# Optimization experiments

Hardware: AMD Instinct MI355X
Metric: run time of the kernel (lower is better)

The kernel has to match this reference:

```python
import jax, jax.numpy as jnp
import numpy as np

B, T, CIN = 64, 1024, 1
H1, H2 = 128, 256  # hidden sizes hardcoded in the flax module


def setup_inputs() -> dict:
    key = jax.random.key(0)
    ks = jax.random.split(key, 24)
    n = lambda k, shp: jax.random.normal(k, shp, dtype=jnp.float32) * 0.05
    z = lambda shp: jnp.zeros(shp, jnp.float32)
    return {
        "X": n(ks[0], (B, T, CIN)),
        "conv_w": n(ks[1], (4, CIN, 16)), "conv_b": z((16,)),
        # gate layout: [i, f, g, o] concatenated, as in flax LSTMCell
        "Wi1": n(ks[2], (16, 4 * H1)), "Wh1": n(ks[3], (H1, 4 * H1)), "b1": z((4 * H1,)),
        "Wi2": n(ks[4], (16, 4 * H1)), "Wh2": n(ks[5], (H1, 4 * H1)), "b2": z((4 * H1,)),
        "Wi3": n(ks[6], (2 * H1, 4 * H2)), "Wh3": n(ks[7], (H2, 4 * H2)), "b3": z((4 * H2,)),
        "Wi4": n(ks[8], (2 * H1, 4 * H2)), "Wh4": n(ks[9], (H2, 4 * H2)), "b4": z((4 * H2,)),
        "attW": n(ks[10], (2 * H2, 128)), "attWb": z((128,)),
        "attV": n(ks[11], (128, 1)), "attVb": z((1,)),
        "d1W": n(ks[12], (2 * H2, 128)), "d1b": z((128,)),
        "d2W": n(ks[13], (128, 1)), "d2b": z((1,)),
    }


def _lstm(x, Wi, Wh, b, hidden):
    """Forward-in-time LSTM over x:(B,T,D) -> outputs (B,T,hidden). flax gate order i,f,g,o."""
    Bb = x.shape[0]

    def step(carry, xt):
        c, h = carry
        z = xt @ Wi + h @ Wh + b  # (B, 4H)
        i, f, g, o = jnp.split(z, 4, axis=-1)
        c = jax.nn.sigmoid(f) * c + jax.nn.sigmoid(i) * jnp.tanh(g)
        h = jax.nn.sigmoid(o) * jnp.tanh(c)
        return (c, h), h

    init = (jnp.zeros((Bb, hidden), x.dtype), jnp.zeros((Bb, hidden), x.dtype))
    _, hs = jax.lax.scan(step, init, jnp.swapaxes(x, 0, 1))  # (T,B,H)
    return jnp.swapaxes(hs, 0, 1)


def reference(X, conv_w, conv_b, Wi1, Wh1, b1, Wi2, Wh2, b2, Wi3, Wh3, b3,
              Wi4, Wh4, b4, attW, attWb, attV, attVb, d1W, d1b, d2W, d2b):
    # Conv1d, SAME padding (flax default)
    x = jax.lax.conv_general_dilated(X, conv_w, (1,), 'SAME',
                                     dimension_numbers=('NWC', 'WIO', 'NWC')) + conv_b
    # NOTE: original flips the FEATURE axis (axis=-1), not time — reproduced faithfully
    x1 = _lstm(x, Wi1, Wh1, b1, H1)
    x2 = _lstm(jnp.flip(x, axis=-1), Wi2, Wh2, b2, H1)
    x = jnp.concatenate([x1, x2], axis=-1)  # (B,T,256)
    x3 = _lstm(x, Wi3, Wh3, b3, H2)
    x4 = _lstm(jnp.flip(x, axis=-1), Wi4, Wh4, b4, H2)
    enc = jnp.concatenate([x3, x4], axis=-1)  # (B,T,512)
    # attention pooling over time
    score = jnp.tanh(enc @ attW + attWb) @ attV + attVb  # (B,T,1)
    w = jax.nn.softmax(score, axis=1)
    ctx = jnp.sum(w * enc, axis=1)  # (B,512)
    h = jnp.tanh(ctx @ d1W + d1b)  # dropout deterministic -> identity
    return h @ d2W + d2b  # (B,1)
```

## Files before the change

kernel.cpp:

```cpp
#include <hip/hip_runtime.h>
#include <hip/hip_fp16.h>

#define B_   64
#define T_   1024
#define H1_  128
#define H2_  256
#define TC_  128
#define NCH  (T_ / TC_)
#define MCH  (B_ * TC_)

typedef unsigned int  u32;
typedef unsigned short u16;
typedef _Float16 half2_t __attribute__((ext_vector_type(2)));
typedef _Float16 half8 __attribute__((ext_vector_type(8)));
typedef float f32x4 __attribute__((ext_vector_type(4)));

__device__ __forceinline__ float fdot2(u32 w, u32 h, float acc) {
    return __builtin_amdgcn_fdot2(__builtin_bit_cast(half2_t, w),
                                  __builtin_bit_cast(half2_t, h), acc, false);
}
__device__ __forceinline__ u32 pk2(float a, float b) {
    __half2 h = __floats2half2_rn(a, b);
    return __builtin_bit_cast(u32, h);
}
__device__ __forceinline__ float hf(u16 u) { return __half2float(__builtin_bit_cast(__half, u)); }
__device__ __forceinline__ u16 fh(float f) { return __builtin_bit_cast(u16, __float2half(f)); }
__device__ __forceinline__ float sigf(float x) { return 1.0f / (1.0f + expf(-x)); }

__global__ void cvt_all(const float* __restrict__ Wh3, const float* __restrict__ Wh4,
                        const float* __restrict__ Wi3, const float* __restrict__ Wi4,
                        const float* __restrict__ attW,
                        const float* __restrict__ Wh1, const float* __restrict__ Wh2,
                        const float* __restrict__ cw, const float* __restrict__ cb,
                        const float* __restrict__ Wi1, const float* __restrict__ Wi2,
                        const float* __restrict__ b1, const float* __restrict__ b2,
                        u32* __restrict__ wpk, u32* __restrict__ wi3T,
                        u32* __restrict__ wi4T, u32* __restrict__ awT,
                        uint4* __restrict__ wpkT, u32* __restrict__ whs,
                        float* __restrict__ w4s, float* __restrict__ beffs)
{
    int idx = blockIdx.x * 256 + threadIdx.x;
    if (idx < 262144) {
        int l = idx >> 17, rem = idx & 131071, k2 = rem >> 10, j = rem & 1023;
        const float* W = l ? Wh4 : Wh3;
        wpk[idx] = pk2(W[(2 * k2) * 1024 + j], W[(2 * k2 + 1) * 1024 + j]);
    } else if (idx < 393216) {
        int rel = idx - 262144, n = rel >> 7, kp = rel & 127;
        wi3T[rel] = pk2(Wi3[(2 * kp) * 1024 + n], Wi3[(2 * kp + 1) * 1024 + n]);
    } else if (idx < 524288) {
        int rel = idx - 393216, n = rel >> 7, kp = rel & 127;
        wi4T[rel] = pk2(Wi4[(255 - 2 * kp) * 1024 + n], Wi4[(254 - 2 * kp) * 1024 + n]);
    } else if (idx < 557056) {
        int rel = idx - 524288, n = rel >> 8, kp = rel & 255;
        awT[rel] = pk2(attW[(2 * kp) * 128 + n], attW[(2 * kp + 1) * 128 + n]);
    } else if (idx < 585728) {
        int rel = idx - 557056;
        int l = rel / 14336;
        int rem = rel - l * 14336;
        int q = rem >> 10, col = rem & 1023;
        const float* W = l ? Wh4 : Wh3;
        int k2 = 72 + 4 * q;
        uint4 v;
        v.x = pk2(W[(2 * k2 + 0) * 1024 + col], W[(2 * k2 + 1) * 1024 + col]);
        v.y = pk2(W[(2 * k2 + 2) * 1024 + col], W[(2 * k2 + 3) * 1024 + col]);
        v.z = pk2(W[(2 * k2 + 4) * 1024 + col], W[(2 * k2 + 5) * 1024 + col]);
        v.w = pk2(W[(2 * k2 + 6) * 1024 + col], W[(2 * k2 + 7) * 1024 + col]);
        wpkT[rel] = v;
    } else if (idx < 651264) {
        int rel = idx - 585728;
        int l = rel >> 15, rem = rel & 32767, p = rem >> 9, col = rem & 511;
        const float* W = l ? Wh2 : Wh1;
        whs[rel] = pk2(W[(2 * p) * 512 + col], W[(2 * p + 1) * 512 + col]);
    } else if (idx < 652288) {
        int rel = idx - 651264;
        int l = rel >> 9, col = rel & 511;
        const float* Wi = l ? Wi2 : Wi1;
        const float* bb = l ? b2 : b1;
#pragma unroll
        for (int kk = 0; kk < 4; ++kk) {
            float s = 0.f;
#pragma unroll
            for (int c0 = 0; c0 < 16; ++c0) {
                int cc = l ? (15 - c0) : c0;
                s += cw[kk * 16 + c0] * Wi[cc * 512 + col];
            }
            w4s[(l * 4 + kk) * 512 + col] = s;
        }
        float be = bb[col];
#pragma unroll
        for (int c0 = 0; c0 < 16; ++c0) {
            int cc = l ? (15 - c0) : c0;
            be += cb[c0] * Wi[cc * 512 + col];
        }
        beffs[l * 512 + col] = be;
    }
}

__global__ __launch_bounds__(512) void fused_step(
    const u16* __restrict__ pre, const u32* __restrict__ wpk,
    const uint4* __restrict__ wpkT, float* __restrict__ state,
    u16* __restrict__ enc,
    const float* __restrict__ X, const u32* __restrict__ whs,
    const float* __restrict__ w4s, const float* __restrict__ beffs,
    float* __restrict__ sstC, u16* __restrict__ sstH,
    u16* __restrict__ x12, int c)
{
    __shared__ __align__(16) uint4 wlA[9][512];
    __shared__ __align__(16) uint4 wlB[9][512];
    __shared__ __align__(16) u32 hbuf_pk[128];
    __shared__ float zbuf[1024];
    __shared__ __align__(16) u32 hbs[64];

    const int j = threadIdx.x;

    if (blockIdx.x < 128) {
        if (c == 0) return;
        const int t0 = (c - 1) * TC_;
        const int blk = blockIdx.x;
        const int b = blk >> 1;
        const int layer = blk & 1;

        const u32* wp = wpk + (size_t)layer * 131072;
        u32 wrA[36], wrB[36];
#pragma unroll
        for (int q = 0; q < 36; ++q) {
            wrA[q] = wp[q * 1024 + j];
            wrB[q] = wp[q * 1024 + 512 + j];
        }
#pragma unroll
        for (int m = 0; m < 9; ++m) {
            uint4 va, vb;
            va.x = wp[(36 + 4 * m + 0) * 1024 + j];
            va.y = wp[(36 + 4 * m + 1) * 1024 + j];
            va.z = wp[(36 + 4 * m + 2) * 1024 + j];
            va.w = wp[(36 + 4 * m + 3) * 1024 + j];
            vb.x = wp[(36 + 4 * m + 0) * 1024 + 512 + j];
            vb.y = wp[(36 + 4 * m + 1) * 1024 + 512 + j];
            vb.z = wp[(36 + 4 * m + 2) * 1024 + 512 + j];
            vb.w = wp[(36 + 4 * m + 3) * 1024 + 512 + j];
            wlA[m][j] = va;
            wlB[m][j] = vb;
        }
        const uint4* wt = wpkT + (size_t)layer * 14 * 1024;

        float* st = state + ((size_t)layer * B_ + b) * 512;
        u16* hb16 = (u16*)hbuf_pk;
        float c_state = 0.f, h_last = 0.f;
        if (j < 256) {
            float h0 = (t0 == 0) ? 0.f : st[256 + j];
            c_state = (t0 == 0) ? 0.f : st[j];
            hb16[j] = fh(h0);
            h_last = h0;
        }
        __syncthreads();

        const u16* prow = pre + (size_t)(layer * MCH + b * TC_) * 1024;
        u16* encrow = enc + ((size_t)b * T_ + t0) * 512 + layer * 256;
        const uint4* hp4 = (const uint4*)hbuf_pk;

        for (int tt = 0; tt < TC_; ++tt, prow += 1024, encrow += 512) {
            u16 pA = prow[j], pB = prow[512 + j];
            float a0 = 0.f, a1 = 0.f, b0 = 0.f, b1 = 0.f;
#pragma unroll
            for (int m = 0; m < 9; ++m) {
                uint4 hh = hp4[m];
                a0 = fdot2(wrA[4 * m + 0], hh.x, a0);
                a1 = fdot2(wrA[4 * m + 1], hh.y, a1);
                a0 = fdot2(wrA[4 * m + 2], hh.z, a0);
                a1 = fdot2(wrA[4 * m + 3], hh.w, a1);
                b0 = fdot2(wrB[4 * m + 0], hh.x, b0);
                b1 = fdot2(wrB[4 * m + 1], hh.y, b1);
                b0 = fdot2(wrB[4 * m + 2], hh.z, b0);
                b1 = fdot2(wrB[4 * m + 3], hh.w, b1);
            }
#pragma unroll
            for (int m = 0; m < 9; ++m) {
                uint4 hh = hp4[9 + m];
                uint4 wa = wlA[m][j];
                uint4 wb = wlB[m][j];
                a0 = fdot2(wa.x, hh.x, a0); a1 = fdot2(wa.y, hh.y, a1);
                a0 = fdot2(wa.z, hh.z, a0); a1 = fdot2(wa.w, hh.w, a1);
                b0 = fdot2(wb.x, hh.x, b0); b1 = fdot2(wb.y, hh.y, b1);
                b0 = fdot2(wb.z, hh.z, b0); b1 = fdot2(wb.w, hh.w, b1);
            }
#pragma unroll
            for (int q = 0; q < 14; ++q) {
                uint4 hh = hp4[18 + q];
                uint4 wa = wt[q * 1024 + j];
                uint4 wb = wt[q * 1024 + 512 + j];
                a0 = fdot2(wa.x, hh.x, a0); a1 = fdot2(wa.y, hh.y, a1);
                a0 = fdot2(wa.z, hh.z, a0); a1 = fdot2(wa.w, hh.w, a1);
                b0 = fdot2(wb.x, hh.x, b0); b1 = fdot2(wb.y, hh.y, b1);
                b0 = fdot2(wb.z, hh.z, b0); b1 = fdot2(wb.w, hh.w, b1);
            }
            float zA = (a0 + a1) + hf(pA);
            float zB = (b0 + b1) + hf(pB);
            zbuf[j] = sigf(zA);
            zbuf[512 + j] = (j < 256) ? tanhf(zB) : sigf(zB);
            __syncthreads();
            if (j < 256) {
                float gi = zbuf[j], gf = zbuf[256 + j], gg = zbuf[512 + j], go = zbuf[768 + j];
                c_state = gf * c_state + gi * gg;
                float h = go * tanhf(c_state);
                hb16[j] = fh(h);
                encrow[j] = fh(h);
                h_last = h;
            }
            __syncthreads();
        }
        if (j < 256) { st[j] = c_state; st[256 + j] = h_last; }
    } else {
        if (c >= NCH) return;
        const int chain = blockIdx.x - 128;
        const int b = chain >> 1;
        const int layer = chain & 1;

        float W4[4];
#pragma unroll
        for (int kk = 0; kk < 4; ++kk) W4[kk] = w4s[(layer * 4 + kk) * 512 + j];
        float beff = beffs[layer * 512 + j];
        u32 whp[64];
#pragma unroll
        for (int p = 0; p < 64; ++p) whp[p] = whs[(layer * 64 + p) * 512 + j];

        u16* hb16 = (u16*)hbs;
        float c_state = 0.f;
        if (j < 128) {
            if (c == 0) hb16[j] = 0;
            else { c_state = sstC[chain * 128 + j]; hb16[j] = sstH[chain * 128 + j]; }
        }
        const int t0 = c * TC_;
        const float* Xb = X + (size_t)b * T_;
        float xm1 = (t0 == 0) ? 0.f : Xb[t0 - 1];
        float x0 = Xb[t0], xp1 = Xb[t0 + 1], xp2 = Xb[t0 + 2];
        __syncthreads();

        const uint4* hp4 = (const uint4*)hbs;
        u16 hprev = 0;
        for (int t = t0; t < t0 + TC_; ++t) {
            float xnext = (t + 3 < T_) ? Xb[t + 3] : 0.f;

            float za = beff + xm1 * W4[0] + x0 * W4[1] + xp1 * W4[2] + xp2 * W4[3];
            float zb = 0.f, zc = 0.f, zd = 0.f;
#pragma unroll
            for (int m = 0; m < 16; ++m) {
                uint4 hh = hp4[m];
                za = fdot2(whp[4 * m + 0], hh.x, za);
                zb = fdot2(whp[4 * m + 1], hh.y, zb);
                zc = fdot2(whp[4 * m + 2], hh.z, zc);
                zd = fdot2(whp[4 * m + 3], hh.w, zd);
            }
            float z = (za + zb) + (zc + zd);
            zbuf[j] = (j >= 256 && j < 384) ? tanhf(z) : sigf(z);
            __syncthreads();
            if (j < 128) {
                float gi = zbuf[j], gf = zbuf[128 + j], gg = zbuf[256 + j], go = zbuf[384 + j];
                c_state = gf * c_state + gi * gg;
                float h = go * tanhf(c_state);
                hprev = fh(h);
                hb16[j] = hprev;
                x12[((size_t)b * T_ + t) * 256 + layer * 128 + j] = hprev;
            }
            xm1 = x0; x0 = xp1; xp1 = xp2; xp2 = xnext;
            __syncthreads();
        }
        if (j < 128) { sstC[chain * 128 + j] = c_state; sstH[chain * 128 + j] = hprev; }
    }
}

template<int OUTMODE, int CHUNK, int LAYERED>
__global__ __launch_bounds__(256) void gemm_mfma(
    const u16* __restrict__ A, const u32* __restrict__ B0, const u32* __restrict__ B1,
    const float* __restrict__ bias0, const float* __restrict__ bias1,
    void* __restrict__ outv, int t0, int N, int K)
{
    __shared__ __align__(16) u32 Al[128][20];
    __shared__ __align__(16) u32 Bl[128][20];
    const int tid = threadIdx.x;
    const int bx = blockIdx.x;
    const int layer = LAYERED ? (bx >> 6) : 0;
    const int m0 = LAYERED ? ((bx & 63) * 128) : (bx * 128);
    const int n0 = blockIdx.y * 128;
    const u32* Bpk = layer ? B1 : B0;
    const float* bias = layer ? bias1 : bias0;
    const int K2 = K >> 1;

    const int w = tid >> 6;
    const int lane = tid & 63;
    const int wr = (w >> 1) * 64, wc = (w & 1) * 64;
    const int lr = lane & 15, lg = lane >> 4;

    f32x4 acc[4][4];
#pragma unroll
    for (int r = 0; r < 4; ++r)
#pragma unroll
        for (int c = 0; c < 4; ++c) acc[r][c] = (f32x4){0.f, 0.f, 0.f, 0.f};

    for (int k0 = 0; k0 < K; k0 += 32) {
        const int kp0 = k0 >> 1;
#pragma unroll
        for (int it = 0; it < 2; ++it) {
            int idx = tid + it * 256;
            int row = idx >> 2, q = idx & 3;
            int grow = m0 + row;
            size_t garow = CHUNK ? ((size_t)(grow >> 7) * T_ + t0 + (grow & 127)) : (size_t)grow;
            uint4 ua = *(const uint4*)(A + garow * K + k0 + q * 8);
            *(uint4*)&Al[row][q * 4] = ua;
            uint4 ub = *(const uint4*)(Bpk + (size_t)(n0 + row) * K2 + kp0 + q * 4);
            *(uint4*)&Bl[row][q * 4] = ub;
        }
        __syncthreads();
        half8 bfr[4];
#pragma unroll
        for (int c = 0; c < 4; ++c) {
            const u32* bp = &Bl[wc + c * 16 + lr][0];
            uint2 blo = *(const uint2*)(bp + 2 * lg);
            uint2 bhi = *(const uint2*)(bp + 8 + 2 * lg);
            uint4 bf = make_uint4(blo.x, blo.y, bhi.x, bhi.y);
            bfr[c] = __builtin_bit_cast(half8, bf);
        }
#pragma unroll
        for (int r = 0; r < 4; ++r) {
            const u32* ap = &Al[wr + r * 16 + lr][0];
            uint2 alo = *(const uint2*)(ap + 2 * lg);
            uint2 ahi = *(const uint2*)(ap + 8 + 2 * lg);
            uint4 af = make_uint4(alo.x, alo.y, ahi.x, ahi.y);
            half8 av = __builtin_bit_cast(half8, af);
#pragma unroll
            for (int c = 0; c < 4; ++c)
                acc[r][c] = __builtin_amdgcn_mfma_f32_16x16x32_f16(av, bfr[c], acc[r][c], 0, 0, 0);
        }
        __syncthreads();
    }

    if (OUTMODE == 0) {
        u16* outp = (u16*)outv + (LAYERED ? (size_t)layer * MCH * 1024 : 0);
#pragma unroll
        for (int c = 0; c < 4; ++c) {
            int col = n0 + wc + c * 16 + lr;
            float bvs = bias[col];
#pragma unroll
            for (int r = 0; r < 4; ++r) {
                int orow = m0 + wr + r * 16 + 4 * lg;
#pragma unroll
                for (int i = 0; i < 4; ++i)
                    outp[(size_t)(orow + i) * N + col] = fh(acc[r][c][i] + bvs);
            }
        }
    } else {
        float* outp = (float*)outv;
#pragma unroll
        for (int c = 0; c < 4; ++c) {
            int col = n0 + wc + c * 16 + lr;
            float bvs = bias[col];
#pragma unroll
            for (int r = 0; r < 4; ++r) {
                int orow = m0 + wr + r * 16 + 4 * lg;
#pragma unroll
                for (int i = 0; i < 4; ++i)
                    outp[(size_t)(orow + i) * N + col] = tanhf(acc[r][c][i] + bvs);
            }
        }
    }
}

__global__ __launch_bounds__(256) void attn_head(
    const float* __restrict__ S1, const u16* __restrict__ enc,
    const float* __restrict__ attV, const float* __restrict__ attVb,
    const float* __restrict__ d1W, const float* __restrict__ d1b,
    const float* __restrict__ d2W, const float* __restrict__ d2b,
    float* __restrict__ out)
{
    const int b = blockIdx.x;
    const int tid = threadIdx.x;
    const int lane = tid & 63, w = tid >> 6;

    __shared__ float sb[1024];
    __shared__ float red[32];
    __shared__ __align__(16) float ctx[512];
    __shared__ float h1s[128];

    float av0 = attV[lane], av1 = attV[64 + lane];
    const float* S1b = S1 + (size_t)b * T_ * 128;
    for (int it = 0; it < 256; ++it) {
        int t = it * 4 + w;
        const float* row = S1b + (size_t)t * 128;
        float p = row[lane] * av0 + row[64 + lane] * av1;
#pragma unroll
        for (int off = 32; off > 0; off >>= 1) p += __shfl_down(p, off);
        if (lane == 0) sb[t] = p + attVb[0];
    }
    __syncthreads();

    float mx = -3.0e38f;
#pragma unroll
    for (int q = 0; q < 4; ++q) mx = fmaxf(mx, sb[tid + 256 * q]);
#pragma unroll
    for (int off = 32; off > 0; off >>= 1) mx = fmaxf(mx, __shfl_down(mx, off));
    if (lane == 0) red[w] = mx;
    __syncthreads();
    if (tid == 0) red[8] = fmaxf(fmaxf(red[0], red[1]), fmaxf(red[2], red[3]));
    __syncthreads();
    float bm = red[8];
    float s = 0.f;
#pragma unroll
    for (int q = 0; q < 4; ++q) {
        float e = expf(sb[tid + 256 * q] - bm);
        sb[tid + 256 * q] = e;
        s += e;
    }
#pragma unroll
    for (int off = 32; off > 0; off >>= 1) s += __shfl_down(s, off);
    if (lane == 0) red[16 + w] = s;
    __syncthreads();
    if (tid == 0) red[24] = 1.0f / (red[16] + red[17] + red[18] + red[19]);
    __syncthreads();
    float inv = red[24];
#pragma unroll
    for (int q = 0; q < 4; ++q) sb[tid + 256 * q] *= inv;
    __syncthreads();

    const u16* encb = enc + (size_t)b * T_ * 512;
    float a0 = 0.f, a1 = 0.f;
    for (int t = 0; t < T_; ++t) {
        float wt = sb[t];
        a0 += wt * hf(encb[(size_t)t * 512 + tid]);
        a1 += wt * hf(encb[(size_t)t * 512 + 256 + tid]);
    }
    ctx[tid] = a0;
    ctx[256 + tid] = a1;
    __syncthreads();

    if (tid < 128) {
        float s1 = d1b[tid];
        for (int k = 0; k < 512; ++k) s1 += ctx[k] * d1W[k * 128 + tid];
        h1s[tid] = tanhf(s1);
    }
    __syncthreads();
    if (tid < 128) {
        float p = h1s[tid] * d2W[tid];
#pragma unroll
        for (int off = 32; off > 0; off >>= 1) p += __shfl_down(p, off);
        if ((tid & 63) == 0) red[28 + (tid >> 6)] = p;
    }
    __syncthreads();
    if (tid == 0) out[b] = red[28] + red[29] + d2b[0];
}

extern "C" void kernel_launch(void* const* d_in, const int* in_sizes, int n_in,
                              void* d_out, int out_size, void* d_ws, size_t ws_size,
                              hipStream_t stream)
{
    const float* X    = (const float*)d_in[0];
    const float* cw   = (const float*)d_in[1];
    const float* cb   = (const float*)d_in[2];
    const float* Wi1  = (const float*)d_in[3];
    const float* Wh1  = (const float*)d_in[4];
    const float* b1   = (const float*)d_in[5];
    const float* Wi2  = (const float*)d_in[6];
    const float* Wh2  = (const float*)d_in[7];
    const float* b2   = (const float*)d_in[8];
    const float* Wi3  = (const float*)d_in[9];
    const float* Wh3  = (const float*)d_in[10];
    const float* b3   = (const float*)d_in[11];
    const float* Wi4  = (const float*)d_in[12];
    const float* Wh4  = (const float*)d_in[13];
    const float* b4   = (const float*)d_in[14];
    const float* attW = (const float*)d_in[15];
    const float* attWb= (const float*)d_in[16];
    const float* attV = (const float*)d_in[17];
    const float* attVb= (const float*)d_in[18];
    const float* d1W  = (const float*)d_in[19];
    const float* d1b  = (const float*)d_in[20];
    const float* d2W  = (const float*)d_in[21];
    const float* d2b  = (const float*)d_in[22];
    float* out = (float*)d_out;

    char* w = (char*)d_ws;
    u16*   x12  = (u16*)w;
    u16*   pre  = (u16*)(w + 33554432);
    u16*   enc  = (u16*)(w + 67108864);
    u32*   wpk  = (u32*)(w + 134217728);
    float* state= (float*)(w + 135266304);
    u32*   wi3T = (u32*)(w + 135528448);
    u32*   wi4T = (u32*)(w + 136052736);
    u32*   awT  = (u32*)(w + 136577024);
    uint4* wpkT = (uint4*)(w + 136708096);
    u32*   whs  = (u32*)(w + 137166848);
    float* w4s  = (float*)(w + 137428992);
    float* beffs= (float*)(w + 137445376);
    float* sstC = (float*)(w + 137449472);
    u16*   sstH = (u16*)(w + 137515008);
    float* S1   = (float*)(w + 33554432);

    cvt_all<<<2548, 256, 0, stream>>>(Wh3, Wh4, Wi3, Wi4, attW, Wh1, Wh2, cw, cb,
                                      Wi1, Wi2, b1, b2,
                                      wpk, wi3T, wi4T, awT, wpkT, whs, w4s, beffs);

    for (int c = 0; c <= NCH; ++c) {
        fused_step<<<256, 512, 0, stream>>>(pre, wpk, wpkT, state, enc,
                                            X, whs, w4s, beffs, sstC, sstH, x12, c);
        if (c < NCH)
            gemm_mfma<0, 1, 1><<<dim3(128, 8), 256, 0, stream>>>(
                x12, wi3T, wi4T, b3, b4, pre, c * TC_, 1024, 256);
    }

    gemm_mfma<1, 0, 0><<<dim3(512, 1), 256, 0, stream>>>(
        enc, awT, awT, attWb, attWb, S1, 0, 128, 512);
    attn_head<<<64, 256, 0, stream>>>(S1, enc, attV, attVb, d1W, d1b, d2W, d2b, out);
}
```

Before: 2.110 ms.

## Keep tail recurrent weights in AGPRs instead of reloading from global memory

The layer-3/4 recurrent matvec previously streamed its last 14 k-groups of weights from global memory on every timestep. Those 15 groups (120 dwords per thread) now sit in accumulation registers (AGPRs), loaded once per chunk and read into VGPRs through v_accvgpr_read with double buffering. To make room, four dwords are moved out of the VGPR-resident portion, and the split and packing offsets in the conversion kernel and workspace are adjusted to match. This removes per-step global and L2 weight traffic, at the cost of extra accvgpr read instructions and heavier register pressure that may limit occupancy or cause spills.

```diff
diff --git a/kernel.cpp b/kernel.cpp
--- a/kernel.cpp
+++ b/kernel.cpp
@@ -26,6 +26,9 @@
 __device__ __forceinline__ float hf(u16 u) { return __half2float(__builtin_bit_cast(__half, u)); }
 __device__ __forceinline__ u16 fh(float f) { return __builtin_bit_cast(u16, __float2half(f)); }
 __device__ __forceinline__ float sigf(float x) { return 1.0f / (1.0f + expf(-x)); }
+
+#define AG_RD(dst, idx) asm volatile("v_accvgpr_read_b32 %0, %1" : "=v"(dst) : "a"(ag[idx]))
+#define AG_WR(idx, src) asm volatile("v_accvgpr_write_b32 %0, %1" : "=a"(ag[idx]) : "v"(src))
 
 __global__ void cvt_all(const float* __restrict__ Wh3, const float* __restrict__ Wh4,
                         const float* __restrict__ Wi3, const float* __restrict__ Wi4,
@@ -53,26 +56,26 @@
     } else if (idx < 557056) {
         int rel = idx - 524288, n = rel >> 8, kp = rel & 255;
         awT[rel] = pk2(attW[(2 * kp) * 128 + n], attW[(2 * kp + 1) * 128 + n]);
-    } else if (idx < 585728) {
+    } else if (idx < 587776) {
         int rel = idx - 557056;
-        int l = rel / 14336;
-        int rem = rel - l * 14336;
+        int l = rel / 15360;
+        int rem = rel - l * 15360;
         int q = rem >> 10, col = rem & 1023;
         const float* W = l ? Wh4 : Wh3;
-        int k2 = 72 + 4 * q;
+        int k2 = 68 + 4 * q;
         uint4 v;
         v.x = pk2(W[(2 * k2 + 0) * 1024 + col], W[(2 * k2 + 1) * 1024 + col]);
         v.y = pk2(W[(2 * k2 + 2) * 1024 + col], W[(2 * k2 + 3) * 1024 + col]);
         v.z = pk2(W[(2 * k2 + 4) * 1024 + col], W[(2 * k2 + 5) * 1024 + col]);
         v.w = pk2(W[(2 * k2 + 6) * 1024 + col], W[(2 * k2 + 7) * 1024 + col]);
         wpkT[rel] = v;
-    } else if (idx < 651264) {
-        int rel = idx - 585728;
+    } else if (idx < 653312) {
+        int rel = idx - 587776;
         int l = rel >> 15, rem = rel & 32767, p = rem >> 9, col = rem & 511;
         const float* W = l ? Wh2 : Wh1;
         whs[rel] = pk2(W[(2 * p) * 512 + col], W[(2 * p + 1) * 512 + col]);
-    } else if (idx < 652288) {
-        int rel = idx - 651264;
+    } else if (idx < 654336) {
+        int rel = idx - 653312;
         int l = rel >> 9, col = rel & 511;
         const float* Wi = l ? Wi2 : Wi1;
         const float* bb = l ? b2 : b1;
@@ -121,27 +124,37 @@
         const int layer = blk & 1;
 
         const u32* wp = wpk + (size_t)layer * 131072;
-        u32 wrA[36], wrB[36];
-#pragma unroll
-        for (int q = 0; q < 36; ++q) {
+        u32 wrA[32], wrB[32];
+#pragma unroll
+        for (int q = 0; q < 32; ++q) {
             wrA[q] = wp[q * 1024 + j];
             wrB[q] = wp[q * 1024 + 512 + j];
         }
 #pragma unroll
         for (int m = 0; m < 9; ++m) {
             uint4 va, vb;
-            va.x = wp[(36 + 4 * m + 0) * 1024 + j];
-            va.y = wp[(36 + 4 * m + 1) * 1024 + j];
-            va.z = wp[(36 + 4 * m + 2) * 1024 + j];
-            va.w = wp[(36 + 4 * m + 3) * 1024 + j];
-            vb.x = wp[(36 + 4 * m + 0) * 1024 + 512 + j];
-            vb.y = wp[(36 + 4 * m + 1) * 1024 + 512 + j];
-            vb.z = wp[(36 + 4 * m + 2) * 1024 + 512 + j];
-            vb.w = wp[(36 + 4 * m + 3) * 1024 + 512 + j];
+            va.x = wp[(32 + 4 * m + 0) * 1024 + j];
+            va.y = wp[(32 + 4 * m + 1) * 1024 + j];
+            va.z = wp[(32 + 4 * m + 2) * 1024 + j];
+            va.w = wp[(32 + 4 * m + 3) * 1024 + j];
+            vb.x = wp[(32 + 4 * m + 0) * 1024 + 512 + j];
+            vb.y = wp[(32 + 4 * m + 1) * 1024 + 512 + j];
+            vb.z = wp[(32 + 4 * m + 2) * 1024 + 512 + j];
+            vb.w = wp[(32 + 4 * m + 3) * 1024 + 512 + j];
             wlA[m][j] = va;
             wlB[m][j] = vb;
         }
-        const uint4* wt = wpkT + (size_t)layer * 14 * 1024;
+        const uint4* wt = wpkT + (size_t)layer * 15360;
+        u32 ag[120];
+#pragma unroll
+        for (int q = 0; q < 15; ++q) {
+            uint4 wa = wt[q * 1024 + j];
+            uint4 wb = wt[q * 1024 + 512 + j];
+            AG_WR(q * 8 + 0, wa.x); AG_WR(q * 8 + 1, wa.y);
+            AG_WR(q * 8 + 2, wa.z); AG_WR(q * 8 + 3, wa.w);
+            AG_WR(q * 8 + 4, wb.x); AG_WR(q * 8 + 5, wb.y);
+            AG_WR(q * 8 + 6, wb.z); AG_WR(q * 8 + 7, wb.w);
+        }
 
         float* st = state + ((size_t)layer * B_ + b) * 512;
         u16* hb16 = (u16*)hbuf_pk;
@@ -161,8 +174,11 @@
         for (int tt = 0; tt < TC_; ++tt, prow += 1024, encrow += 512) {
             u16 pA = prow[j], pB = prow[512 + j];
             float a0 = 0.f, a1 = 0.f, b0 = 0.f, b1 = 0.f;
-#pragma unroll
-            for (int m = 0; m < 9; ++m) {
+            u32 wb0[8], wb1[8];
+            AG_RD(wb0[0], 0); AG_RD(wb0[1], 1); AG_RD(wb0[2], 2); AG_RD(wb0[3], 3);
+            AG_RD(wb0[4], 4); AG_RD(wb0[5], 5); AG_RD(wb0[6], 6); AG_RD(wb0[7], 7);
+#pragma unroll
+            for (int m = 0; m < 8; ++m) {
                 uint4 hh = hp4[m];
                 a0 = fdot2(wrA[4 * m + 0], hh.x, a0);
                 a1 = fdot2(wrA[4 * m + 1], hh.y, a1);
@@ -175,7 +191,7 @@
             }
 #pragma unroll
             for (int m = 0; m < 9; ++m) {
-                uint4 hh = hp4[9 + m];
+                uint4 hh = hp4[8 + m];
                 uint4 wa = wlA[m][j];
                 uint4 wb = wlB[m][j];
                 a0 = fdot2(wa.x, hh.x, a0); a1 = fdot2(wa.y, hh.y, a1);
@@ -183,16 +199,33 @@
                 b0 = fdot2(wb.x, hh.x, b0); b1 = fdot2(wb.y, hh.y, b1);
                 b0 = fdot2(wb.z, hh.z, b0); b1 = fdot2(wb.w, hh.w, b1);
             }
-#pragma unroll
-            for (int q = 0; q < 14; ++q) {
-                uint4 hh = hp4[18 + q];
-                uint4 wa = wt[q * 1024 + j];
-                uint4 wb = wt[q * 1024 + 512 + j];
-                a0 = fdot2(wa.x, hh.x, a0); a1 = fdot2(wa.y, hh.y, a1);
-                a0 = fdot2(wa.z, hh.z, a0); a1 = fdot2(wa.w, hh.w, a1);
-                b0 = fdot2(wb.x, hh.x, b0); b1 = fdot2(wb.y, hh.y, b1);
-                b0 = fdot2(wb.z, hh.z, b0); b1 = fdot2(wb.w, hh.w, b1);
-            }
+#define AG_GROUP(CUR, NXT, G)                                                  \
+            do {                                                               \
+                uint4 hh = hp4[17 + (G)];                                      \
+                if ((G) < 14) {                                                \
+                    AG_RD(NXT[0], ((G) + 1) * 8 + 0);                          \
+                    AG_RD(NXT[1], ((G) + 1) * 8 + 1);                          \
+                    AG_RD(NXT[2], ((G) + 1) * 8 + 2);                          \
+                    AG_RD(NXT[3], ((G) + 1) * 8 + 3);                          \
+                    AG_RD(NXT[4], ((G) + 1) * 8 + 4);                          \
+                    AG_RD(NXT[5], ((G) + 1) * 8 + 5);                          \
+                    AG_RD(NXT[6], ((G) + 1) * 8 + 6);                          \
+                    AG_RD(NXT[7], ((G) + 1) * 8 + 7);                          \
+                }                                                              \
+                a0 = fdot2(CUR[0], hh.x, a0); a1 = fdot2(CUR[1], hh.y, a1);    \
+                a0 = fdot2(CUR[2], hh.z, a0); a1 = fdot2(CUR[3], hh.w, a1);    \
+                b0 = fdot2(CUR[4], hh.x, b0); b1 = fdot2(CUR[5], hh.y, b1);    \
+                b0 = fdot2(CUR[6], hh.z, b0); b1 = fdot2(CUR[7], hh.w, b1);    \
+            } while (0)
+            AG_GROUP(wb0, wb1, 0);  AG_GROUP(wb1, wb0, 1);
+            AG_GROUP(wb0, wb1, 2);  AG_GROUP(wb1, wb0, 3);
+            AG_GROUP(wb0, wb1, 4);  AG_GROUP(wb1, wb0, 5);
+            AG_GROUP(wb0, wb1, 6);  AG_GROUP(wb1, wb0, 7);
+            AG_GROUP(wb0, wb1, 8);  AG_GROUP(wb1, wb0, 9);
+            AG_GROUP(wb0, wb1, 10); AG_GROUP(wb1, wb0, 11);
+            AG_GROUP(wb0, wb1, 12); AG_GROUP(wb1, wb0, 13);
+            AG_GROUP(wb0, wb1, 14);
+#undef AG_GROUP
             float zA = (a0 + a1) + hf(pA);
             float zB = (b0 + b1) + hf(pB);
             zbuf[j] = sigf(zA);
@@ -486,14 +519,14 @@
     u32*   wi4T = (u32*)(w + 136052736);
     u32*   awT  = (u32*)(w + 136577024);
     uint4* wpkT = (uint4*)(w + 136708096);
-    u32*   whs  = (u32*)(w + 137166848);
-    float* w4s  = (float*)(w + 137428992);
-    float* beffs= (float*)(w + 137445376);
-    float* sstC = (float*)(w + 137449472);
-    u16*   sstH = (u16*)(w + 137515008);
+    u32*   whs  = (u32*)(w + 137199616);
+    float* w4s  = (float*)(w + 137461760);
+    float* beffs= (float*)(w + 137478144);
+    float* sstC = (float*)(w + 137482240);
+    u16*   sstH = (u16*)(w + 137547776);
     float* S1   = (float*)(w + 33554432);
 
-    cvt_all<<<2548, 256, 0, stream>>>(Wh3, Wh4, Wi3, Wi4, attW, Wh1, Wh2, cw, cb,
+    cvt_all<<<2556, 256, 0, stream>>>(Wh3, Wh4, Wi3, Wi4, attW, Wh1, Wh2, cw, cb,
                                       Wi1, Wi2, b1, b2,
                                       wpk, wi3T, wi4T, awT, wpkT, whs, w4s, beffs);
 
```

Result: slower. 3.179 ms (+50.7%).
